# Performance work log

Hardware: AMD Instinct MI355X
Metric: run time of the kernel (lower is better)

Reference implementation:

```python
import jax, jax.numpy as jnp
import numpy as np

N_USER = 50000
N_ITEM = 50000
N = N_USER + N_ITEM
NNZ = 3200000
EMB = 64
N_LAYERS = 3
BATCH = 4096
NEG_SLOPE = 0.2


def setup_inputs() -> dict:
    key = jax.random.key(0)
    ks = jax.random.split(key, 12)
    inp = {
        "users": jax.random.randint(ks[0], (BATCH,), 0, N_USER),
        "pos_items": jax.random.randint(ks[1], (BATCH,), 0, N_ITEM),
        "neg_items": jax.random.randint(ks[2], (BATCH,), 0, N_ITEM),
        "adj_row": jax.random.randint(ks[3], (NNZ,), 0, N),
        "adj_col": jax.random.randint(ks[4], (NNZ,), 0, N),
        # normalized adjacency values ~ 1/degree scale
        "adj_val": jax.random.uniform(ks[5], (NNZ,), dtype=jnp.float32) * (1.0 / 32.0),
        "user_emb": jax.random.normal(ks[6], (N_USER, EMB), dtype=jnp.float32) * 0.1,
        "item_emb": jax.random.normal(ks[7], (N_ITEM, EMB), dtype=jnp.float32) * 0.1,
        "W_gc": jax.random.normal(ks[8], (N_LAYERS, EMB, EMB), dtype=jnp.float32) * (1.0 / np.sqrt(EMB)),
        "b_gc": jax.random.normal(ks[9], (N_LAYERS, 1, EMB), dtype=jnp.float32) * 0.01,
        "W_bi": jax.random.normal(ks[10], (N_LAYERS, EMB, EMB), dtype=jnp.float32) * (1.0 / np.sqrt(EMB)),
        "b_bi": jax.random.normal(ks[11], (N_LAYERS, 1, EMB), dtype=jnp.float32) * 0.01,
    }
    return inp


def _spmm(adj_row, adj_col, adj_val, x):
    # sparse [N,N] @ dense [N,D] via gather + segment_sum
    msgs = adj_val[:, None] * x[adj_col]            # [nnz, D]
    return jax.ops.segment_sum(msgs, adj_row, num_segments=N)


def reference(users, pos_items, neg_items, adj_row, adj_col, adj_val,
              user_emb, item_emb, W_gc, b_gc, W_bi, b_bi):
    ego = jnp.concatenate([user_emb, item_emb], axis=0)   # [N, EMB]
    all_embs = [ego]
    for k in range(N_LAYERS):
        side = _spmm(adj_row, adj_col, adj_val, ego)      # [N, EMB]
        sum_emb = side @ W_gc[k] + b_gc[k]                # GC transform
        bi_emb = (ego * side) @ W_bi[k] + b_bi[k]         # BI transform
        ego = jax.nn.leaky_relu(sum_emb + bi_emb, negative_slope=NEG_SLOPE)
        # mess_dropout = 0 -> identity; L2 normalize rows (F.normalize, eps=1e-12)
        norm = jnp.maximum(jnp.linalg.norm(ego, axis=1, keepdims=True), 1e-12)
        all_embs.append(ego / norm)
    all_embs = jnp.concatenate(all_embs, axis=1)          # [N, EMB*(L+1)]
    u_g = all_embs[:N_USER]
    i_g = all_embs[N_USER:]
    return (u_g[users], i_g[pos_items], i_g[neg_items])
```

## Files before the change

### kernel.cpp

```cpp
#include <hip/hip_runtime.h>
#include <hip/hip_bf16.h>

#define N_USERC 50000
#define N_ITEMC 50000
#define NTOT    100000
#define NNZC    3200000
#define NGRP    (NNZC/4)
#define EMBC    64
#define BATCHC  4096
#define NSLOT   (3*BATCHC)
#define NBKT    196
#define CAP     17408
typedef unsigned long long u64;

typedef __attribute__((ext_vector_type(4))) float floatx4;
typedef __attribute__((ext_vector_type(2))) float floatx2;
typedef __attribute__((ext_vector_type(4))) int   intx4;
typedef __attribute__((ext_vector_type(2))) int   intx2;
typedef __attribute__((ext_vector_type(2))) unsigned uintx2;
typedef __attribute__((ext_vector_type(8))) short shortx8;

__device__ __forceinline__ float bf2f(unsigned short u) {
    return __int_as_float(((int)u) << 16);
}
__device__ __forceinline__ unsigned short f2bf(float f) {
    __hip_bfloat16 h = __float2bfloat16(f);
    return *(unsigned short*)&h;
}
__device__ __forceinline__ unsigned v2fix(float v) {
    int q = (int)(v * 1048576.0f + 0.5f);
    return (unsigned)min(q, 32767);
}

#define NB_INIT  (NTOT * EMBC / 4 / 256)
#define NB_SCAT  ((NNZC + 4095) / 4096)
__global__ __launch_bounds__(256) void k_prepscat(
    const intx4* __restrict__ row4, const intx4* __restrict__ col4,
    const floatx4* __restrict__ val4, int* __restrict__ gbcur, u64* __restrict__ eb,
    const float4* __restrict__ ue, const float4* __restrict__ ie, ushort4* __restrict__ xb0,
    const float* __restrict__ Wgc, const float* __restrict__ Wbi,
    const float* __restrict__ bgc, const float* __restrict__ bbi,
    unsigned short* __restrict__ wgT, unsigned short* __restrict__ wbT,
    float* __restrict__ biasSum) {
    __shared__ int bh[NBKT], bbase[NBKT], bcur[NBKT];
    __shared__ float wlds[64 * 65];
    int tid = threadIdx.x;
    if (blockIdx.x < NB_SCAT) {
        for (int i = tid; i < NBKT; i += 256) { bh[i] = 0; bcur[i] = 0; }
        __syncthreads();
        long gbase = (long)blockIdx.x * 1024;
        u64 e[16]; int bk[16];
        #pragma unroll
        for (int it = 0; it < 4; ++it) {
            long g = gbase + it * 256 + tid;
            if (g < NGRP) {
                intx4 r = __builtin_nontemporal_load(row4 + g);
                intx4 c = __builtin_nontemporal_load(col4 + g);
                floatx4 v = __builtin_nontemporal_load(val4 + g);
                e[it*4+0] = ((u64)r.x << 32) | ((u64)(unsigned)c.x << 15) | v2fix(v.x); bk[it*4+0] = r.x >> 9;
                e[it*4+1] = ((u64)r.y << 32) | ((u64)(unsigned)c.y << 15) | v2fix(v.y); bk[it*4+1] = r.y >> 9;
                e[it*4+2] = ((u64)r.z << 32) | ((u64)(unsigned)c.z << 15) | v2fix(v.z); bk[it*4+2] = r.z >> 9;
                e[it*4+3] = ((u64)r.w << 32) | ((u64)(unsigned)c.w << 15) | v2fix(v.w); bk[it*4+3] = r.w >> 9;
                atomicAdd(&bh[bk[it*4+0]], 1);
                atomicAdd(&bh[bk[it*4+1]], 1);
                atomicAdd(&bh[bk[it*4+2]], 1);
                atomicAdd(&bh[bk[it*4+3]], 1);
            } else {
                bk[it*4+0] = bk[it*4+1] = bk[it*4+2] = bk[it*4+3] = -1;
            }
        }
        __syncthreads();
        for (int i = tid; i < NBKT; i += 256)
            if (bh[i] > 0) bbase[i] = atomicAdd(&gbcur[i], bh[i]);
        __syncthreads();
        #pragma unroll
        for (int i = 0; i < 16; i++) {
            if (bk[i] >= 0) {
                int p = bk[i] * CAP + bbase[bk[i]] + atomicAdd(&bcur[bk[i]], 1);
                eb[p] = e[i];
            }
        }
    } else if (blockIdx.x < NB_SCAT + NB_INIT) {
        long i = (long)(blockIdx.x - NB_SCAT) * 256 + tid;
        const long nu4 = (long)N_USERC * EMBC / 4;
        float4 v = (i < nu4) ? ue[i] : ie[i - nu4];
        ushort4 b; b.x = f2bf(v.x); b.y = f2bf(v.y); b.z = f2bf(v.z); b.w = f2bf(v.w);
        xb0[i] = b;
    } else {
        int wb = blockIdx.x - NB_SCAT - NB_INIT;
        int k = wb >> 1, m = wb & 1;
        const float* W = (m ? Wbi : Wgc) + k * 4096;
        unsigned short* WT = (m ? wbT : wgT) + k * 4096;
        #pragma unroll
        for (int it = 0; it < 4; ++it) {
            int i = it * 1024 + tid * 4;
            float4 v = *(const float4*)(W + i);
            int d = i >> 6, c = i & 63;
            wlds[d * 65 + c + 0] = v.x;
            wlds[d * 65 + c + 1] = v.y;
            wlds[d * 65 + c + 2] = v.z;
            wlds[d * 65 + c + 3] = v.w;
        }
        __syncthreads();
        int c = tid >> 2;
        int d0 = (tid & 3) * 16;
        unsigned short vals[16];
        #pragma unroll
        for (int j = 0; j < 16; ++j)
            vals[j] = f2bf(wlds[(d0 + j) * 65 + c]);
        *(uint4*)(WT + tid * 16)     = *(const uint4*)(vals);
        *(uint4*)(WT + tid * 16 + 8) = *(const uint4*)(vals + 8);
        if (m == 0 && tid < 64) biasSum[k * 64 + tid] = bgc[k * 64 + tid] + bbi[k * 64 + tid];
    }
}

__global__ __launch_bounds__(1024) void k_csrC(const u64* __restrict__ eb, const int* __restrict__ gbcur,
                                               intx2* __restrict__ rp2, unsigned* __restrict__ ecv) {
    __shared__ int lhist[512];
    __shared__ int lcur[512];
    __shared__ int sm[256];
    int b = blockIdx.x;
    int tid = threadIdx.x;
    int row0 = b << 9;
    if (tid < 512) lhist[tid] = 0;
    __syncthreads();
    int start = b * CAP;
    int end = start + gbcur[b];
    for (int e = start + tid; e < end; e += 1024) {
        u64 w = eb[e];
        int rl = (int)((w >> 32) & 0x1FFFF) - row0;
        atomicAdd(&lhist[rl], 1);
    }
    __syncthreads();
    int h0 = 0, h1 = 0, pair = 0;
    if (tid < 256) {
        h0 = lhist[2 * tid]; h1 = lhist[2 * tid + 1];
        pair = h0 + h1;
        sm[tid] = pair;
    }
    __syncthreads();
    for (int off = 1; off < 256; off <<= 1) {
        int u = 0;
        if (tid < 256 && tid >= off) u = sm[tid - off];
        __syncthreads();
        if (tid < 256) sm[tid] += u;
        __syncthreads();
    }
    if (tid < 256) {
        int pairExcl = sm[tid] - pair;
        int e0 = start + pairExcl;
        int e1 = e0 + h0;
        lcur[2 * tid] = e0;
        lcur[2 * tid + 1] = e1;
        int rg0 = row0 + 2 * tid, rg1 = rg0 + 1;
        if (rg0 < NTOT) { intx2 v; v.x = e0; v.y = e1; rp2[rg0] = v; }
        if (rg1 < NTOT) { intx2 v; v.x = e1; v.y = e1 + h1; rp2[rg1] = v; }
    }
    __syncthreads();
    for (int e = start + tid; e < end; e += 1024) {
        u64 w = eb[e];
        int rl = (int)((w >> 32) & 0x1FFFF) - row0;
        int p = atomicAdd(&lcur[rl], 1);
        ecv[p] = (unsigned)(w & 0xFFFFFFFFu);
    }
}

#define SPMM_BLOCKS 2048
__global__ __launch_bounds__(256) void k_spmm(const intx2* __restrict__ rp2, const unsigned* __restrict__ ecv,
                                              const unsigned short* __restrict__ xb,
                                              unsigned short* __restrict__ side_bf) {
    int wid = blockIdx.x * 4 + (threadIdx.x >> 6);
    int lane = threadIdx.x & 63;
    int q = lane >> 4;
    int t4 = (lane & 15) * 4;
    unsigned tb = (unsigned)(t4 * 2);
    const char* xbc = (const char*)xb;
    for (int r = wid; r < NTOT; r += SPMM_BLOCKS * 4) {
        intx2 se = rp2[r];
        int s = se.x;
        int len = se.y - s;
        const unsigned* ebase = ecv + s;
        floatx2 acc01 = {0.f, 0.f}, acc23 = {0.f, 0.f};

        int nfull = len >> 4;
        int j = 0;
        for (int it = 0; it < nfull; ++it, j += 16) {
            unsigned pk[4];
            #pragma unroll
            for (int u = 0; u < 4; ++u)
                pk[u] = __builtin_nontemporal_load(ebase + j + u * 4 + q);
            uintx2 xv[4];
            #pragma unroll
            for (int u = 0; u < 4; ++u)
                xv[u] = *(const uintx2*)(xbc + ((pk[u] >> 15) * 128u + tb));
            #pragma unroll
            for (int u = 0; u < 4; ++u) {
                float w = (float)(pk[u] & 0x7fffu);
                floatx2 x01, x23;
                x01.x = __uint_as_float(xv[u].x << 16);
                x01.y = __uint_as_float(xv[u].x & 0xffff0000u);
                x23.x = __uint_as_float(xv[u].y << 16);
                x23.y = __uint_as_float(xv[u].y & 0xffff0000u);
                acc01 += w * x01;
                acc23 += w * x23;
            }
        }
        if (j < len) {
            unsigned pk[4]; bool vm[4];
            #pragma unroll
            for (int u = 0; u < 4; ++u) {
                int je = j + u * 4 + q;
                vm[u] = (je < len);
                pk[u] = __builtin_nontemporal_load(ebase + (vm[u] ? je : 0));
            }
            uintx2 xv[4];
            #pragma unroll
            for (int u = 0; u < 4; ++u)
                xv[u] = *(const uintx2*)(xbc + ((pk[u] >> 15) * 128u + tb));
            #pragma unroll
            for (int u = 0; u < 4; ++u) {
                float w = vm[u] ? (float)(pk[u] & 0x7fffu) : 0.f;
                floatx2 x01, x23;
                x01.x = __uint_as_float(xv[u].x << 16);
                x01.y = __uint_as_float(xv[u].x & 0xffff0000u);
                x23.x = __uint_as_float(xv[u].y << 16);
                x23.y = __uint_as_float(xv[u].y & 0xffff0000u);
                acc01 += w * x01;
                acc23 += w * x23;
            }
        }

        float a0 = acc01.x, a1 = acc01.y, a2 = acc23.x, a3 = acc23.y;
        a0 += __shfl_xor(a0, 16); a1 += __shfl_xor(a1, 16); a2 += __shfl_xor(a2, 16); a3 += __shfl_xor(a3, 16);
        a0 += __shfl_xor(a0, 32); a1 += __shfl_xor(a1, 32); a2 += __shfl_xor(a2, 32); a3 += __shfl_xor(a3, 32);
        if (lane < 16) {
            const float SC = 1.0f / 1048576.0f;
            ushort4 o; o.x = f2bf(a0 * SC); o.y = f2bf(a1 * SC); o.z = f2bf(a2 * SC); o.w = f2bf(a3 * SC);
            *(ushort4*)(side_bf + (long)r * EMBC + t4) = o;
        }
    }
}

#define RPB 128
#define LDP 72
__global__ __launch_bounds__(256) void k_layer_mfma(
    const unsigned short* __restrict__ side_bf, const unsigned short* __restrict__ xb_in,
    unsigned short* __restrict__ xb_out,
    const unsigned short* __restrict__ wgT, const unsigned short* __restrict__ wbT,
    const float* __restrict__ biasSum)
{
    __shared__ unsigned short sS[RPB * LDP];
    __shared__ unsigned short sM[RPB * LDP];
    __shared__ unsigned short sWg[64 * LDP];
    __shared__ unsigned short sWb[64 * LDP];
    __shared__ float sBias[64];

    int tid = threadIdx.x;
    int row0 = blockIdx.x * RPB;

    #pragma unroll
    for (int it = 0; it < 2; ++it) {
        int item = it * 256 + tid;
        int c = item >> 3, ch = item & 7;
        *(uint4*)(sWg + c * LDP + ch * 8) = *(const uint4*)(wgT + c * 64 + ch * 8);
        *(uint4*)(sWb + c * LDP + ch * 8) = *(const uint4*)(wbT + c * 64 + ch * 8);
    }
    if (tid < 64) sBias[tid] = biasSum[tid];

    #pragma unroll
    for (int it = 0; it < (RPB * 8) / 256; ++it) {
        int item = it * 256 + tid;
        int r = item >> 3, ch = item & 7;
        long grow = row0 + r;
        uint4 sv = make_uint4(0, 0, 0, 0), ev = make_uint4(0, 0, 0, 0);
        if (grow < NTOT) {
            sv = *(const uint4*)(side_bf + grow * 64 + ch * 8);
            ev = *(const uint4*)(xb_in + grow * 64 + ch * 8);
        }
        uint4 mv;
        mv.x = f2bf(bf2f(ev.x & 0xffff) * bf2f(sv.x & 0xffff)) |
               ((unsigned int)f2bf(bf2f(ev.x >> 16) * bf2f(sv.x >> 16)) << 16);
        mv.y = f2bf(bf2f(ev.y & 0xffff) * bf2f(sv.y & 0xffff)) |
               ((unsigned int)f2bf(bf2f(ev.y >> 16) * bf2f(sv.y >> 16)) << 16);
        mv.z = f2bf(bf2f(ev.z & 0xffff) * bf2f(sv.z & 0xffff)) |
               ((unsigned int)f2bf(bf2f(ev.z >> 16) * bf2f(sv.z >> 16)) << 16);
        mv.w = f2bf(bf2f(ev.w & 0xffff) * bf2f(sv.w & 0xffff)) |
               ((unsigned int)f2bf(bf2f(ev.w >> 16) * bf2f(sv.w >> 16)) << 16);
        *(uint4*)(sS + r * LDP + ch * 8) = sv;
        *(uint4*)(sM + r * LDP + ch * 8) = mv;
    }
    __syncthreads();

    int wave = tid >> 6, lane = tid & 63;
    int quad = lane >> 4, l16 = lane & 15;

    floatx4 accG[2][4], accB[2][4];
    #pragma unroll
    for (int rt = 0; rt < 2; rt++)
        #pragma unroll
        for (int ct = 0; ct < 4; ct++) {
            accG[rt][ct] = (floatx4){0.f, 0.f, 0.f, 0.f};
            accB[rt][ct] = (floatx4){0.f, 0.f, 0.f, 0.f};
        }

    #pragma unroll
    for (int kc = 0; kc < 64; kc += 32) {
        shortx8 aS[2], aM[2];
        #pragma unroll
        for (int rt = 0; rt < 2; rt++) {
            int r = wave * 32 + rt * 16 + l16;
            aS[rt] = *(const shortx8*)(sS + r * LDP + kc + quad * 8);
            aM[rt] = *(const shortx8*)(sM + r * LDP + kc + quad * 8);
        }
        #pragma unroll
        for (int ct = 0; ct < 4; ct++) {
            int c = ct * 16 + l16;
            shortx8 bG = *(const shortx8*)(sWg + c * LDP + kc + quad * 8);
            shortx8 bB = *(const shortx8*)(sWb + c * LDP + kc + quad * 8);
            #pragma unroll
            for (int rt = 0; rt < 2; rt++) {
                accG[rt][ct] = __builtin_amdgcn_mfma_f32_16x16x32_bf16(aS[rt], bG, accG[rt][ct], 0, 0, 0);
                accB[rt][ct] = __builtin_amdgcn_mfma_f32_16x16x32_bf16(aM[rt], bB, accB[rt][ct], 0, 0, 0);
            }
        }
    }

    #pragma unroll
    for (int rt = 0; rt < 2; rt++)
        #pragma unroll
        for (int ct = 0; ct < 4; ct++) {
            int c = ct * 16 + l16;
            float bs = sBias[c];
            #pragma unroll
            for (int reg = 0; reg < 4; reg++) {
                int r = wave * 32 + rt * 16 + quad * 4 + reg;
                long grow = row0 + r;
                if (grow < NTOT) {
                    float v = accG[rt][ct][reg] + accB[rt][ct][reg] + bs;
                    float o = (v > 0.f) ? v : 0.2f * v;
                    xb_out[grow * 64 + c] = f2bf(o);
                }
            }
        }
}

__global__ __launch_bounds__(256) void k_gatherAll(
    const unsigned short* __restrict__ xb0, const unsigned short* __restrict__ xb1,
    const unsigned short* __restrict__ xb2, const unsigned short* __restrict__ xb3,
    const int* __restrict__ users, const int* __restrict__ pos, const int* __restrict__ neg,
    float* __restrict__ out) {
    int gw = (blockIdx.x * blockDim.x + threadIdx.x) >> 6;
    int lane = threadIdx.x & 63;
    int slot = gw >> 2, layer = gw & 3;
    if (slot >= NSLOT) return;
    int row;
    if (slot < BATCHC)          row = users[slot];
    else if (slot < 2 * BATCHC) row = N_USERC + pos[slot - BATCHC];
    else                        row = N_USERC + neg[slot - 2 * BATCHC];
    const unsigned short* src = (layer == 0) ? xb0 : (layer == 1) ? xb1 : (layer == 2) ? xb2 : xb3;
    float v = bf2f(src[(long)row * 64 + lane]);
    if (layer != 0) {
        float ss = v * v;
        for (int off = 32; off > 0; off >>= 1) ss += __shfl_xor(ss, off);
        float nrm = fmaxf(sqrtf(ss), 1e-12f);
        v = v / nrm;
    }
    out[(long)slot * 256 + layer * 64 + lane] = v;
}

extern "C" void kernel_launch(void* const* d_in, const int* in_sizes, int n_in,
                              void* d_out, int out_size, void* d_ws, size_t ws_size,
                              hipStream_t stream) {
    const int*   users   = (const int*)d_in[0];
    const int*   pos     = (const int*)d_in[1];
    const int*   neg     = (const int*)d_in[2];
    const int*   adj_row = (const int*)d_in[3];
    const int*   adj_col = (const int*)d_in[4];
    const float* adj_val = (const float*)d_in[5];
    const float* user_emb = (const float*)d_in[6];
    const float* item_emb = (const float*)d_in[7];
    const float* W_gc = (const float*)d_in[8];
    const float* b_gc = (const float*)d_in[9];
    const float* W_bi = (const float*)d_in[10];
    const float* b_bi = (const float*)d_in[11];
    float* out = (float*)d_out;

    char* p = (char*)d_ws;
    unsigned* ecv = (unsigned*)p;               p += (size_t)NBKT * CAP * 4;
    u64*  eb  = (u64*)p;                        p += (size_t)NBKT * CAP * 8;
    unsigned short* xb2 = (unsigned short*)eb;
    unsigned short* xb3 = (unsigned short*)((char*)eb + (size_t)NTOT * EMBC * 2);
    unsigned short* side_bf = (unsigned short*)p; p += (size_t)NTOT * EMBC * 2;
    unsigned short* xb0 = (unsigned short*)p;   p += (size_t)NTOT * EMBC * 2;
    unsigned short* xb1 = (unsigned short*)p;   p += (size_t)NTOT * EMBC * 2;
    intx2* rp2 = (intx2*)p;                     p += (size_t)NTOT * 8;
    int*  gbcur = (int*)p;                      p += 1024;
    unsigned short* wgT = (unsigned short*)p;   p += 3 * 4096 * 2;
    unsigned short* wbT = (unsigned short*)p;   p += 3 * 4096 * 2;
    float* biasSum = (float*)p;                 p += 3 * 64 * 4;

    hipMemsetAsync(gbcur, 0, 1024, stream);

    k_prepscat<<<NB_SCAT + NB_INIT + 6, 256, 0, stream>>>(
        (const intx4*)adj_row, (const intx4*)adj_col, (const floatx4*)adj_val, gbcur, eb,
        (const float4*)user_emb, (const float4*)item_emb, (ushort4*)xb0,
        W_gc, W_bi, b_gc, b_bi, wgT, wbT, biasSum);

    k_csrC<<<NBKT, 1024, 0, stream>>>(eb, gbcur, rp2, ecv);

    unsigned short* xbs[4] = {xb0, xb1, xb2, xb3};
    const int NB_LAYER = (NTOT + RPB - 1) / RPB;
    for (int k = 0; k < 3; k++) {
        k_spmm<<<SPMM_BLOCKS, 256, 0, stream>>>(rp2, ecv, xbs[k], side_bf);
        k_layer_mfma<<<NB_LAYER, 256, 0, stream>>>(side_bf, xbs[k], xbs[k + 1],
            wgT + (size_t)k * 4096, wbT + (size_t)k * 4096, biasSum + (size_t)k * 64);
    }
    k_gatherAll<<<(NSLOT * 4) / 4, 256, 0, stream>>>(xb0, xb1, xb2, xb3, users, pos, neg, out);
}
```

Measured before the change: 394.3 us.

## Fuse SpMM aggregation with MFMA layer transform into one per-layer kernel

Merges the sparse aggregation and the dense GC/BI transform into a single kernel. Each wave aggregates 16 rows into shared memory, then runs the MFMA transform on them directly. This removes the side_bf round trip through global memory and one launch per layer. In exchange, the grid-stride SpMM launch becomes a fixed 1563-block grid, and weights are read from global memory rather than staged in LDS. Per-wave row imbalance could also hurt load balance.

```diff
diff --git a/kernel.cpp b/kernel.cpp
--- a/kernel.cpp
+++ b/kernel.cpp
@@ -165,118 +165,99 @@
     }
 }
 
-#define SPMM_BLOCKS 2048
-__global__ __launch_bounds__(256) void k_spmm(const intx2* __restrict__ rp2, const unsigned* __restrict__ ecv,
-                                              const unsigned short* __restrict__ xb,
-                                              unsigned short* __restrict__ side_bf) {
-    int wid = blockIdx.x * 4 + (threadIdx.x >> 6);
-    int lane = threadIdx.x & 63;
-    int q = lane >> 4;
-    int t4 = (lane & 15) * 4;
+#define LBLK 64
+#define NLB  1563
+#define LDP  72
+__global__ __launch_bounds__(256) void k_layer(
+    const intx2* __restrict__ rp2, const unsigned* __restrict__ ecv,
+    const unsigned short* __restrict__ xb_in, unsigned short* __restrict__ xb_out,
+    const unsigned short* __restrict__ wgT, const unsigned short* __restrict__ wbT,
+    const float* __restrict__ biasSum)
+{
+    __shared__ unsigned short sS[LBLK * LDP];
+    __shared__ unsigned short sM[LBLK * LDP];
+    int tid = threadIdx.x;
+    int wv = tid >> 6, lane = tid & 63, q = lane >> 4, l16 = lane & 15;
+    int wrow0 = blockIdx.x * LBLK + wv * 16;
+    int t4 = l16 * 4;
     unsigned tb = (unsigned)(t4 * 2);
-    const char* xbc = (const char*)xb;
-    for (int r = wid; r < NTOT; r += SPMM_BLOCKS * 4) {
-        intx2 se = rp2[r];
-        int s = se.x;
-        int len = se.y - s;
-        const unsigned* ebase = ecv + s;
+    const char* xbc = (const char*)xb_in;
+
+    for (int rr = 0; rr < 16; ++rr) {
+        int r = wrow0 + rr;
         floatx2 acc01 = {0.f, 0.f}, acc23 = {0.f, 0.f};
-
-        int nfull = len >> 4;
-        int j = 0;
-        for (int it = 0; it < nfull; ++it, j += 16) {
-            unsigned pk[4];
-            #pragma unroll
-            for (int u = 0; u < 4; ++u)
-                pk[u] = __builtin_nontemporal_load(ebase + j + u * 4 + q);
-            uintx2 xv[4];
-            #pragma unroll
-            for (int u = 0; u < 4; ++u)
-                xv[u] = *(const uintx2*)(xbc + ((pk[u] >> 15) * 128u + tb));
-            #pragma unroll
-            for (int u = 0; u < 4; ++u) {
-                float w = (float)(pk[u] & 0x7fffu);
-                floatx2 x01, x23;
-                x01.x = __uint_as_float(xv[u].x << 16);
-                x01.y = __uint_as_float(xv[u].x & 0xffff0000u);
-                x23.x = __uint_as_float(xv[u].y << 16);
-                x23.y = __uint_as_float(xv[u].y & 0xffff0000u);
-                acc01 += w * x01;
-                acc23 += w * x23;
-            }
-        }
-        if (j < len) {
-            unsigned pk[4]; bool vm[4];
-            #pragma unroll
-            for (int u = 0; u < 4; ++u) {
-                int je = j + u * 4 + q;
-                vm[u] = (je < len);
-                pk[u] = __builtin_nontemporal_load(ebase + (vm[u] ? je : 0));
-            }
-            uintx2 xv[4];
-            #pragma unroll
-            for (int u = 0; u < 4; ++u)
-                xv[u] = *(const uintx2*)(xbc + ((pk[u] >> 15) * 128u + tb));
-            #pragma unroll
-            for (int u = 0; u < 4; ++u) {
-                float w = vm[u] ? (float)(pk[u] & 0x7fffu) : 0.f;
-                floatx2 x01, x23;
-                x01.x = __uint_as_float(xv[u].x << 16);
-                x01.y = __uint_as_float(xv[u].x & 0xffff0000u);
-                x23.x = __uint_as_float(xv[u].y << 16);
-                x23.y = __uint_as_float(xv[u].y & 0xffff0000u);
-                acc01 += w * x01;
-                acc23 += w * x23;
-            }
-        }
-
+        if (r < NTOT) {
+            intx2 se = rp2[r];
+            int s = se.x;
+            int len = se.y - s;
+            const unsigned* ebase = ecv + s;
+            int nfull = len >> 4;
+            int j = 0;
+            for (int it = 0; it < nfull; ++it, j += 16) {
+                unsigned pk[4];
+                #pragma unroll
+                for (int u = 0; u < 4; ++u)
+                    pk[u] = __builtin_nontemporal_load(ebase + j + u * 4 + q);
+                uintx2 xv[4];
+                #pragma unroll
+                for (int u = 0; u < 4; ++u)
+                    xv[u] = *(const uintx2*)(xbc + ((pk[u] >> 15) * 128u + tb));
+                #pragma unroll
+                for (int u = 0; u < 4; ++u) {
+                    float w = (float)(pk[u] & 0x7fffu);
+                    floatx2 x01, x23;
+                    x01.x = __uint_as_float(xv[u].x << 16);
+                    x01.y = __uint_as_float(xv[u].x & 0xffff0000u);
+                    x23.x = __uint_as_float(xv[u].y << 16);
+                    x23.y = __uint_as_float(xv[u].y & 0xffff0000u);
+                    acc01 += w * x01;
+                    acc23 += w * x23;
+                }
+            }
+            if (j < len) {
+                unsigned pk[4]; bool vm[4];
+                #pragma unroll
+                for (int u = 0; u < 4; ++u) {
+                    int je = j + u * 4 + q;
+                    vm[u] = (je < len);
+                    pk[u] = __builtin_nontemporal_load(ebase + (vm[u] ? je : 0));
+                }
+                uintx2 xv[4];
+                #pragma unroll
+                for (int u = 0; u < 4; ++u)
+                    xv[u] = *(const uintx2*)(xbc + ((pk[u] >> 15) * 128u + tb));
+                #pragma unroll
+                for (int u = 0; u < 4; ++u) {
+                    float w = vm[u] ? (float)(pk[u] & 0x7fffu) : 0.f;
+                    floatx2 x01, x23;
+                    x01.x = __uint_as_float(xv[u].x << 16);
+                    x01.y = __uint_as_float(xv[u].x & 0xffff0000u);
+                    x23.x = __uint_as_float(xv[u].y << 16);
+                    x23.y = __uint_as_float(xv[u].y & 0xffff0000u);
+                    acc01 += w * x01;
+                    acc23 += w * x23;
+                }
+            }
+        }
         float a0 = acc01.x, a1 = acc01.y, a2 = acc23.x, a3 = acc23.y;
         a0 += __shfl_xor(a0, 16); a1 += __shfl_xor(a1, 16); a2 += __shfl_xor(a2, 16); a3 += __shfl_xor(a3, 16);
         a0 += __shfl_xor(a0, 32); a1 += __shfl_xor(a1, 32); a2 += __shfl_xor(a2, 32); a3 += __shfl_xor(a3, 32);
         if (lane < 16) {
             const float SC = 1.0f / 1048576.0f;
             ushort4 o; o.x = f2bf(a0 * SC); o.y = f2bf(a1 * SC); o.z = f2bf(a2 * SC); o.w = f2bf(a3 * SC);
-            *(ushort4*)(side_bf + (long)r * EMBC + t4) = o;
-        }
-    }
-}
-
-#define RPB 128
-#define LDP 72
-__global__ __launch_bounds__(256) void k_layer_mfma(
-    const unsigned short* __restrict__ side_bf, const unsigned short* __restrict__ xb_in,
-    unsigned short* __restrict__ xb_out,
-    const unsigned short* __restrict__ wgT, const unsigned short* __restrict__ wbT,
-    const float* __restrict__ biasSum)
-{
-    __shared__ unsigned short sS[RPB * LDP];
-    __shared__ unsigned short sM[RPB * LDP];
-    __shared__ unsigned short sWg[64 * LDP];
-    __shared__ unsigned short sWb[64 * LDP];
-    __shared__ float sBias[64];
-
-    int tid = threadIdx.x;
-    int row0 = blockIdx.x * RPB;
+            *(ushort4*)(sS + (wv * 16 + rr) * LDP + t4) = o;
+        }
+    }
 
     #pragma unroll
     for (int it = 0; it < 2; ++it) {
-        int item = it * 256 + tid;
-        int c = item >> 3, ch = item & 7;
-        *(uint4*)(sWg + c * LDP + ch * 8) = *(const uint4*)(wgT + c * 64 + ch * 8);
-        *(uint4*)(sWb + c * LDP + ch * 8) = *(const uint4*)(wbT + c * 64 + ch * 8);
-    }
-    if (tid < 64) sBias[tid] = biasSum[tid];
-
-    #pragma unroll
-    for (int it = 0; it < (RPB * 8) / 256; ++it) {
-        int item = it * 256 + tid;
-        int r = item >> 3, ch = item & 7;
-        long grow = row0 + r;
-        uint4 sv = make_uint4(0, 0, 0, 0), ev = make_uint4(0, 0, 0, 0);
-        if (grow < NTOT) {
-            sv = *(const uint4*)(side_bf + grow * 64 + ch * 8);
-            ev = *(const uint4*)(xb_in + grow * 64 + ch * 8);
-        }
+        int item = it * 64 + lane;
+        int rr = item >> 3, ch = item & 7;
+        int r = wrow0 + rr;
+        int lr = wv * 16 + rr;
+        uint4 sv = *(const uint4*)(sS + lr * LDP + ch * 8);
+        uint4 ev = make_uint4(0, 0, 0, 0);
+        if (r < NTOT) ev = *(const uint4*)(xb_in + (long)r * 64 + ch * 8);
         uint4 mv;
         mv.x = f2bf(bf2f(ev.x & 0xffff) * bf2f(sv.x & 0xffff)) |
                ((unsigned int)f2bf(bf2f(ev.x >> 16) * bf2f(sv.x >> 16)) << 16);
@@ -286,62 +267,43 @@
                ((unsigned int)f2bf(bf2f(ev.z >> 16) * bf2f(sv.z >> 16)) << 16);
         mv.w = f2bf(bf2f(ev.w & 0xffff) * bf2f(sv.w & 0xffff)) |
                ((unsigned int)f2bf(bf2f(ev.w >> 16) * bf2f(sv.w >> 16)) << 16);
-        *(uint4*)(sS + r * LDP + ch * 8) = sv;
-        *(uint4*)(sM + r * LDP + ch * 8) = mv;
-    }
-    __syncthreads();
-
-    int wave = tid >> 6, lane = tid & 63;
-    int quad = lane >> 4, l16 = lane & 15;
-
-    floatx4 accG[2][4], accB[2][4];
+        *(uint4*)(sM + lr * LDP + ch * 8) = mv;
+    }
+
+    floatx4 accG[4], accB[4];
     #pragma unroll
-    for (int rt = 0; rt < 2; rt++)
-        #pragma unroll
-        for (int ct = 0; ct < 4; ct++) {
-            accG[rt][ct] = (floatx4){0.f, 0.f, 0.f, 0.f};
-            accB[rt][ct] = (floatx4){0.f, 0.f, 0.f, 0.f};
-        }
-
+    for (int ct = 0; ct < 4; ct++) {
+        accG[ct] = (floatx4){0.f, 0.f, 0.f, 0.f};
+        accB[ct] = (floatx4){0.f, 0.f, 0.f, 0.f};
+    }
     #pragma unroll
     for (int kc = 0; kc < 64; kc += 32) {
-        shortx8 aS[2], aM[2];
-        #pragma unroll
-        for (int rt = 0; rt < 2; rt++) {
-            int r = wave * 32 + rt * 16 + l16;
-            aS[rt] = *(const shortx8*)(sS + r * LDP + kc + quad * 8);
-            aM[rt] = *(const shortx8*)(sM + r * LDP + kc + quad * 8);
-        }
+        int lr = wv * 16 + l16;
+        shortx8 aS = *(const shortx8*)(sS + lr * LDP + kc + q * 8);
+        shortx8 aM = *(const shortx8*)(sM + lr * LDP + kc + q * 8);
         #pragma unroll
         for (int ct = 0; ct < 4; ct++) {
             int c = ct * 16 + l16;
-            shortx8 bG = *(const shortx8*)(sWg + c * LDP + kc + quad * 8);
-            shortx8 bB = *(const shortx8*)(sWb + c * LDP + kc + quad * 8);
-            #pragma unroll
-            for (int rt = 0; rt < 2; rt++) {
-                accG[rt][ct] = __builtin_amdgcn_mfma_f32_16x16x32_bf16(aS[rt], bG, accG[rt][ct], 0, 0, 0);
-                accB[rt][ct] = __builtin_amdgcn_mfma_f32_16x16x32_bf16(aM[rt], bB, accB[rt][ct], 0, 0, 0);
-            }
-        }
-    }
-
+            shortx8 bG = *(const shortx8*)(wgT + c * 64 + kc + q * 8);
+            shortx8 bB = *(const shortx8*)(wbT + c * 64 + kc + q * 8);
+            accG[ct] = __builtin_amdgcn_mfma_f32_16x16x32_bf16(aS, bG, accG[ct], 0, 0, 0);
+            accB[ct] = __builtin_amdgcn_mfma_f32_16x16x32_bf16(aM, bB, accB[ct], 0, 0, 0);
+        }
+    }
     #pragma unroll
-    for (int rt = 0; rt < 2; rt++)
-        #pragma unroll
-        for (int ct = 0; ct < 4; ct++) {
-            int c = ct * 16 + l16;
-            float bs = sBias[c];
-            #pragma unroll
-            for (int reg = 0; reg < 4; reg++) {
-                int r = wave * 32 + rt * 16 + quad * 4 + reg;
-                long grow = row0 + r;
-                if (grow < NTOT) {
-                    float v = accG[rt][ct][reg] + accB[rt][ct][reg] + bs;
-                    float o = (v > 0.f) ? v : 0.2f * v;
-                    xb_out[grow * 64 + c] = f2bf(o);
-                }
-            }
-        }
+    for (int ct = 0; ct < 4; ct++) {
+        int c = ct * 16 + l16;
+        float bs = biasSum[c];
+        #pragma unroll
+        for (int reg = 0; reg < 4; reg++) {
+            int r = wrow0 + q * 4 + reg;
+            if (r < NTOT) {
+                float v = accG[ct][reg] + accB[ct][reg] + bs;
+                float o = (v > 0.f) ? v : 0.2f * v;
+                xb_out[(long)r * 64 + c] = f2bf(o);
+            }
+        }
+    }
 }
 
 __global__ __launch_bounds__(256) void k_gatherAll(
@@ -398,6 +360,7 @@
     unsigned short* wgT = (unsigned short*)p;   p += 3 * 4096 * 2;
     unsigned short* wbT = (unsigned short*)p;   p += 3 * 4096 * 2;
     float* biasSum = (float*)p;                 p += 3 * 64 * 4;
+    (void)side_bf;
 
     hipMemsetAsync(gbcur, 0, 1024, stream);
 
@@ -409,10 +372,8 @@
     k_csrC<<<NBKT, 1024, 0, stream>>>(eb, gbcur, rp2, ecv);
 
     unsigned short* xbs[4] = {xb0, xb1, xb2, xb3};
-    const int NB_LAYER = (NTOT + RPB - 1) / RPB;
     for (int k = 0; k < 3; k++) {
-        k_spmm<<<SPMM_BLOCKS, 256, 0, stream>>>(rp2, ecv, xbs[k], side_bf);
-        k_layer_mfma<<<NB_LAYER, 256, 0, stream>>>(side_bf, xbs[k], xbs[k + 1],
+        k_layer<<<NLB, 256, 0, stream>>>(rp2, ecv, xbs[k], xbs[k + 1],
             wgT + (size_t)k * 4096, wbT + (size_t)k * 4096, biasSum + (size_t)k * 64);
     }
     k_gatherAll<<<(NSLOT * 4) / 4, 256, 0, stream>>>(xb0, xb1, xb2, xb3, users, pos, neg, out);
```

After: 549.9 us. 39.5% more time.

## Quantize SpMM gather input to per-row int8 with float scales

Applied to the files above, without the earlier changes.

Adds a per-row symmetric int8 copy (offset by 128) and a per-row float scale for each layer's input embeddings, written by the init path and by the layer kernel epilogue. The SpMM now gathers 4 bytes per lane instead of 8, plus one scale per edge, and subtracts the offset through a running sum of weights. The aim is to halve the bytes of the random gathers that dominate SpMM, at the cost of extra quantization work, an extra scale load per edge, and lower precision in the aggregated messages.

```diff
diff --git a/kernel.cpp b/kernel.cpp
--- a/kernel.cpp
+++ b/kernel.cpp
@@ -38,6 +38,7 @@
     const intx4* __restrict__ row4, const intx4* __restrict__ col4,
     const floatx4* __restrict__ val4, int* __restrict__ gbcur, u64* __restrict__ eb,
     const float4* __restrict__ ue, const float4* __restrict__ ie, ushort4* __restrict__ xb0,
+    unsigned* __restrict__ xq0, float* __restrict__ scl0,
     const float* __restrict__ Wgc, const float* __restrict__ Wbi,
     const float* __restrict__ bgc, const float* __restrict__ bbi,
     unsigned short* __restrict__ wgT, unsigned short* __restrict__ wbT,
@@ -86,6 +87,18 @@
         float4 v = (i < nu4) ? ue[i] : ie[i - nu4];
         ushort4 b; b.x = f2bf(v.x); b.y = f2bf(v.y); b.z = f2bf(v.z); b.w = f2bf(v.w);
         xb0[i] = b;
+        float m = fmaxf(fmaxf(fabsf(v.x), fabsf(v.y)), fmaxf(fabsf(v.z), fabsf(v.w)));
+        m = fmaxf(m, __shfl_xor(m, 1));
+        m = fmaxf(m, __shfl_xor(m, 2));
+        m = fmaxf(m, __shfl_xor(m, 4));
+        m = fmaxf(m, __shfl_xor(m, 8));
+        float inv = (m > 0.f) ? 127.0f / m : 0.f;
+        unsigned u0 = (unsigned)(int)rintf(v.x * inv + 128.0f);
+        unsigned u1 = (unsigned)(int)rintf(v.y * inv + 128.0f);
+        unsigned u2 = (unsigned)(int)rintf(v.z * inv + 128.0f);
+        unsigned u3 = (unsigned)(int)rintf(v.w * inv + 128.0f);
+        xq0[i] = u0 | (u1 << 8) | (u2 << 16) | (u3 << 24);
+        if ((tid & 15) == 0) scl0[i >> 4] = m * (1.0f / 127.0f);
     } else {
         int wb = blockIdx.x - NB_SCAT - NB_INIT;
         int k = wb >> 1, m = wb & 1;
@@ -167,20 +180,19 @@
 
 #define SPMM_BLOCKS 2048
 __global__ __launch_bounds__(256) void k_spmm(const intx2* __restrict__ rp2, const unsigned* __restrict__ ecv,
-                                              const unsigned short* __restrict__ xb,
+                                              const unsigned* __restrict__ xq, const float* __restrict__ scl,
                                               unsigned short* __restrict__ side_bf) {
     int wid = blockIdx.x * 4 + (threadIdx.x >> 6);
     int lane = threadIdx.x & 63;
     int q = lane >> 4;
     int t4 = (lane & 15) * 4;
-    unsigned tb = (unsigned)(t4 * 2);
-    const char* xbc = (const char*)xb;
+    const char* xqc = (const char*)xq;
     for (int r = wid; r < NTOT; r += SPMM_BLOCKS * 4) {
         intx2 se = rp2[r];
         int s = se.x;
         int len = se.y - s;
         const unsigned* ebase = ecv + s;
-        floatx2 acc01 = {0.f, 0.f}, acc23 = {0.f, 0.f};
+        float a0 = 0.f, a1 = 0.f, a2 = 0.f, a3 = 0.f, cs = 0.f;
 
         int nfull = len >> 4;
         int j = 0;
@@ -189,20 +201,21 @@
             #pragma unroll
             for (int u = 0; u < 4; ++u)
                 pk[u] = __builtin_nontemporal_load(ebase + j + u * 4 + q);
-            uintx2 xv[4];
-            #pragma unroll
-            for (int u = 0; u < 4; ++u)
-                xv[u] = *(const uintx2*)(xbc + ((pk[u] >> 15) * 128u + tb));
+            unsigned xv[4]; float sc[4];
             #pragma unroll
             for (int u = 0; u < 4; ++u) {
-                float w = (float)(pk[u] & 0x7fffu);
-                floatx2 x01, x23;
-                x01.x = __uint_as_float(xv[u].x << 16);
-                x01.y = __uint_as_float(xv[u].x & 0xffff0000u);
-                x23.x = __uint_as_float(xv[u].y << 16);
-                x23.y = __uint_as_float(xv[u].y & 0xffff0000u);
-                acc01 += w * x01;
-                acc23 += w * x23;
+                unsigned col = pk[u] >> 15;
+                xv[u] = *(const unsigned*)(xqc + (col * 64u + t4));
+                sc[u] = scl[col];
+            }
+            #pragma unroll
+            for (int u = 0; u < 4; ++u) {
+                float ws = (float)(pk[u] & 0x7fffu) * sc[u];
+                cs += ws;
+                a0 += ws * (float)(xv[u] & 0xffu);
+                a1 += ws * (float)((xv[u] >> 8) & 0xffu);
+                a2 += ws * (float)((xv[u] >> 16) & 0xffu);
+                a3 += ws * (float)(xv[u] >> 24);
             }
         }
         if (j < len) {
@@ -213,24 +226,26 @@
                 vm[u] = (je < len);
                 pk[u] = __builtin_nontemporal_load(ebase + (vm[u] ? je : 0));
             }
-            uintx2 xv[4];
-            #pragma unroll
-            for (int u = 0; u < 4; ++u)
-                xv[u] = *(const uintx2*)(xbc + ((pk[u] >> 15) * 128u + tb));
+            unsigned xv[4]; float sc[4];
             #pragma unroll
             for (int u = 0; u < 4; ++u) {
-                float w = vm[u] ? (float)(pk[u] & 0x7fffu) : 0.f;
-                floatx2 x01, x23;
-                x01.x = __uint_as_float(xv[u].x << 16);
-                x01.y = __uint_as_float(xv[u].x & 0xffff0000u);
-                x23.x = __uint_as_float(xv[u].y << 16);
-                x23.y = __uint_as_float(xv[u].y & 0xffff0000u);
-                acc01 += w * x01;
-                acc23 += w * x23;
-            }
-        }
-
-        float a0 = acc01.x, a1 = acc01.y, a2 = acc23.x, a3 = acc23.y;
+                unsigned col = pk[u] >> 15;
+                xv[u] = *(const unsigned*)(xqc + (col * 64u + t4));
+                sc[u] = scl[col];
+            }
+            #pragma unroll
+            for (int u = 0; u < 4; ++u) {
+                float ws = vm[u] ? (float)(pk[u] & 0x7fffu) * sc[u] : 0.f;
+                cs += ws;
+                a0 += ws * (float)(xv[u] & 0xffu);
+                a1 += ws * (float)((xv[u] >> 8) & 0xffu);
+                a2 += ws * (float)((xv[u] >> 16) & 0xffu);
+                a3 += ws * (float)(xv[u] >> 24);
+            }
+        }
+
+        float c128 = 128.0f * cs;
+        a0 -= c128; a1 -= c128; a2 -= c128; a3 -= c128;
         a0 += __shfl_xor(a0, 16); a1 += __shfl_xor(a1, 16); a2 += __shfl_xor(a2, 16); a3 += __shfl_xor(a3, 16);
         a0 += __shfl_xor(a0, 32); a1 += __shfl_xor(a1, 32); a2 += __shfl_xor(a2, 32); a3 += __shfl_xor(a3, 32);
         if (lane < 16) {
@@ -246,6 +261,7 @@
 __global__ __launch_bounds__(256) void k_layer_mfma(
     const unsigned short* __restrict__ side_bf, const unsigned short* __restrict__ xb_in,
     unsigned short* __restrict__ xb_out,
+    unsigned char* __restrict__ xq_out, float* __restrict__ scl_out,
     const unsigned short* __restrict__ wgT, const unsigned short* __restrict__ wbT,
     const float* __restrict__ biasSum)
 {
@@ -325,6 +341,7 @@
         }
     }
 
+    float ov[2][4][4];
     #pragma unroll
     for (int rt = 0; rt < 2; rt++)
         #pragma unroll
@@ -333,15 +350,46 @@
             float bs = sBias[c];
             #pragma unroll
             for (int reg = 0; reg < 4; reg++) {
-                int r = wave * 32 + rt * 16 + quad * 4 + reg;
-                long grow = row0 + r;
-                if (grow < NTOT) {
-                    float v = accG[rt][ct][reg] + accB[rt][ct][reg] + bs;
-                    float o = (v > 0.f) ? v : 0.2f * v;
-                    xb_out[grow * 64 + c] = f2bf(o);
+                float v = accG[rt][ct][reg] + accB[rt][ct][reg] + bs;
+                ov[rt][ct][reg] = (v > 0.f) ? v : 0.2f * v;
+            }
+        }
+    #pragma unroll
+    for (int rt = 0; rt < 2; rt++)
+        #pragma unroll
+        for (int ct = 0; ct < 4; ct++) {
+            int c = ct * 16 + l16;
+            #pragma unroll
+            for (int reg = 0; reg < 4; reg++) {
+                long grow = row0 + wave * 32 + rt * 16 + quad * 4 + reg;
+                if (grow < NTOT) xb_out[grow * 64 + c] = f2bf(ov[rt][ct][reg]);
+            }
+        }
+    if (xq_out != nullptr) {
+        #pragma unroll
+        for (int rt = 0; rt < 2; rt++) {
+            #pragma unroll
+            for (int reg = 0; reg < 4; reg++) {
+                float m = fmaxf(fmaxf(fabsf(ov[rt][0][reg]), fabsf(ov[rt][1][reg])),
+                                fmaxf(fabsf(ov[rt][2][reg]), fabsf(ov[rt][3][reg])));
+                m = fmaxf(m, __shfl_xor(m, 1));
+                m = fmaxf(m, __shfl_xor(m, 2));
+                m = fmaxf(m, __shfl_xor(m, 4));
+                m = fmaxf(m, __shfl_xor(m, 8));
+                float inv = (m > 0.f) ? 127.0f / m : 0.f;
+                int r = row0 + wave * 32 + rt * 16 + quad * 4 + reg;
+                #pragma unroll
+                for (int ct = 0; ct < 4; ct++) {
+                    int c = ct * 16 + l16;
+                    if (r < NTOT) {
+                        int u = (int)rintf(ov[rt][ct][reg] * inv) + 128;
+                        xq_out[(long)r * 64 + c] = (unsigned char)u;
+                    }
                 }
-            }
-        }
+                if (l16 == 0 && r < NTOT) scl_out[r] = m * (1.0f / 127.0f);
+            }
+        }
+    }
 }
 
 __global__ __launch_bounds__(256) void k_gatherAll(
@@ -398,21 +446,31 @@
     unsigned short* wgT = (unsigned short*)p;   p += 3 * 4096 * 2;
     unsigned short* wbT = (unsigned short*)p;   p += 3 * 4096 * 2;
     float* biasSum = (float*)p;                 p += 3 * 64 * 4;
+    unsigned char* xqA = (unsigned char*)p;     p += (size_t)NTOT * EMBC;
+    unsigned char* xqB = (unsigned char*)p;     p += (size_t)NTOT * EMBC;
+    float* sclA = (float*)p;                    p += (size_t)NTOT * 4;
+    float* sclB = (float*)p;                    p += (size_t)NTOT * 4;
 
     hipMemsetAsync(gbcur, 0, 1024, stream);
 
     k_prepscat<<<NB_SCAT + NB_INIT + 6, 256, 0, stream>>>(
         (const intx4*)adj_row, (const intx4*)adj_col, (const floatx4*)adj_val, gbcur, eb,
         (const float4*)user_emb, (const float4*)item_emb, (ushort4*)xb0,
+        (unsigned*)xqA, sclA,
         W_gc, W_bi, b_gc, b_bi, wgT, wbT, biasSum);
 
     k_csrC<<<NBKT, 1024, 0, stream>>>(eb, gbcur, rp2, ecv);
 
     unsigned short* xbs[4] = {xb0, xb1, xb2, xb3};
+    unsigned char* xqin[3]  = {xqA, xqB, xqA};
+    float*         sclin[3] = {sclA, sclB, sclA};
+    unsigned char* xqout[3]  = {xqB, xqA, nullptr};
+    float*         sclout[3] = {sclB, sclA, nullptr};
     const int NB_LAYER = (NTOT + RPB - 1) / RPB;
     for (int k = 0; k < 3; k++) {
-        k_spmm<<<SPMM_BLOCKS, 256, 0, stream>>>(rp2, ecv, xbs[k], side_bf);
+        k_spmm<<<SPMM_BLOCKS, 256, 0, stream>>>(rp2, ecv, (const unsigned*)xqin[k], sclin[k], side_bf);
         k_layer_mfma<<<NB_LAYER, 256, 0, stream>>>(side_bf, xbs[k], xbs[k + 1],
+            xqout[k], sclout[k],
             wgT + (size_t)k * 4096, wbT + (size_t)k * 4096, biasSum + (size_t)k * 64);
     }
     k_gatherAll<<<(NSLOT * 4) / 4, 256, 0, stream>>>(xb0, xb1, xb2, xb3, users, pos, neg, out);
```

After: 429.6 us. 1.09x slower.
